# Kernel optimization log

Measured on AMD Instinct MI355X. Metric: run time of the kernel, lower is better.

The kernel has to match this reference:

```python
import jax, jax.numpy as jnp
import numpy as np


def _conv3d(x, w):
    # x: [N, C, D, H, W], w: [O, I, K, K, K] -> [N, O, D', H', W'] VALID conv
    return jax.lax.conv_general_dilated(
        x, w, window_strides=(1, 1, 1), padding='VALID',
        dimension_numbers=('NCDHW', 'OIDHW', 'NCDHW'))


def conv4d(x, w):
    # x: [B, C, D1, D2, D3, D4]; w: [O, I, K1, K2, K3, K4]
    # Decompose 4D conv as a sum over K1 taps of 3D convs; the sliced D1
    # window is folded into the batch dimension so XLA's 3D conv does the work.
    B, C, D1, D2, D3, D4 = x.shape
    O, I, K1, K2, K3, K4 = w.shape
    D1o = D1 - K1 + 1
    out = None
    for i in range(K1):  # small fixed loop over kernel taps (K1=3)
        xs = jax.lax.dynamic_slice_in_dim(x, i, D1o, axis=2)      # [B,C,D1o,D2,D3,D4]
        xs = xs.transpose(0, 2, 1, 3, 4, 5).reshape(B * D1o, C, D2, D3, D4)
        y = _conv3d(xs, w[:, :, i])                                # [B*D1o,O,d2,d3,d4]
        out = y if out is None else out + y
    d2, d3, d4 = out.shape[2], out.shape[3], out.shape[4]
    out = out.reshape(B, D1o, O, d2, d3, d4).transpose(0, 2, 1, 3, 4, 5)
    return out  # [B, O, D1o, d2, d3, d4]


def setup_inputs() -> dict:
    key = jax.random.key(0)
    k1, k2 = jax.random.split(key)
    pic_in = jax.random.normal(k1, (2, 16, 8, 8, 64, 64), dtype=jnp.float32)
    # convNd weight: [out_channels, in_channels, K, K, K, K], no bias
    weight = jax.random.normal(k2, (32, 16, 3, 3, 3, 3), dtype=jnp.float32) * 0.05
    return {"pic_in": pic_in, "weight": weight}


def reference(pic_in, weight):
    # ConvKernel.forward: 4D conv (stride 1, padding 0, no bias) + ReLU
    return jax.nn.relu(conv4d(pic_in, weight))
```

## Files before the change

### kernel.cpp

```cpp
#include <hip/hip_runtime.h>


typedef __attribute__((ext_vector_type(8))) __bf16 bf16x8;
typedef __attribute__((ext_vector_type(16))) float f32x16;

#define CSTRIDE 262144

#define WT_OFF 0
#define XB_OFF 131072
#define BUF_STRIDE 12544

typedef __attribute__((address_space(1))) const unsigned int gu32;
typedef __attribute__((address_space(3))) unsigned int lu32;

__device__ __forceinline__ void async_cp16(const void* g, void* l) {
  __builtin_amdgcn_global_load_lds((gu32*)g, (lu32*)l, 16, 0, 0);
}

__global__ __launch_bounds__(256) void prep(const float* __restrict__ x,
                                            const float* __restrict__ w,
                                            unsigned char* __restrict__ ws) {
  int blk = blockIdx.x;
  if (blk < 512) {
    __bf16* xb = (__bf16*)(ws + XB_OFF);
    int n = blk * 256 + threadIdx.x;
    int cg = n & 15;
    int d3 = (n >> 4) & 63;
    int d2 = (n >> 10) & 7;
    int d1 = (n >> 13) & 7;
    int b = n >> 16;
    const float* gx =
        x + ((((b * 16) * 8 + d1) * 8 + d2) * 64 + d3) * 64 + cg * 4;
    float4 v[16];
#pragma unroll
    for (int c = 0; c < 16; ++c) v[c] = *(const float4*)(gx + (size_t)c * CSTRIDE);
    __bf16* row = xb + ((((b * 8 + d1) * 8 + d2) * 64 + d3) * 1024);
#pragma unroll
    for (int ch = 0; ch < 2; ++ch) {
#pragma unroll
      for (int j = 0; j < 4; ++j) {
        bf16x8 o;
#pragma unroll
        for (int cc = 0; cc < 8; ++cc)
          o[cc] = (__bf16)(((const float*)&v[ch * 8 + cc])[j]);
        *(bf16x8*)(row + ch * 512 + (cg * 4 + j) * 8) = o;
      }
    }
  } else {
    int o = blk - 512;
    __bf16* wT = (__bf16*)(ws + WT_OFF);
#pragma unroll
    for (int base = 0; base < 1296; base += 256) {
      int idx = base + threadIdx.x;
      if (idx < 1296) {
        int c = idx / 81, t = idx % 81;
        wT[t * 512 + o * 16 + c] = (__bf16)w[o * 1296 + idx];
      }
    }
  }
}

__global__ __launch_bounds__(256, 4) void conv_mfma(
    const unsigned char* __restrict__ ws, float* __restrict__ out) {
  const __bf16* wT = (const __bf16*)(ws + WT_OFF);
  const unsigned char* xb = ws + XB_OFF;

  int bid = blockIdx.x;
  int c3 = bid & 15;
  int t = bid >> 4;
  int e2 = t % 6;
  t /= 6;
  int e1 = t % 6;
  int b = t / 6;
  int r0 = c3 * 4;
  int T3 = (c3 == 15) ? 2 : 4;
  int nchunk = (T3 + 2) * 2;
  int ntiles = T3 >> 1;

  int lane = threadIdx.x & 63;
  int wave = threadIdx.x >> 6;
  int m32 = lane & 31;
  int half = lane >> 5;

  __shared__ __align__(16) unsigned char lds[2 * BUF_STRIDE];

  int ab_off = (wave >> 1) * 2048 + half * 1024 + ((wave & 1) * 32 + m32) * 16;

  f32x16 acc[2];
#pragma unroll
  for (int i = 0; i < 2; ++i)
#pragma unroll
    for (int r = 0; r < 16; ++r) acc[i][r] = 0.f;

  {
    const unsigned char* g =
        xb + (((b * 8 + e1) * 8 + e2) * 64 + r0) * 2048;
#pragma unroll
    for (int j = 0; j < 3; ++j) {
      int ck = j * 4 + wave;
      if (ck < nchunk) async_cp16(g + ck * 1024 + lane * 16, lds + ck * 1024);
    }
  }

  for (int p = 0; p < 9; ++p) {
    __syncthreads();
    const __bf16* wp = wT + p * 4608 + m32 * 16 + half * 8;
    bf16x8 bfr[9];
#pragma unroll
    for (int t9 = 0; t9 < 9; ++t9) bfr[t9] = *(const bf16x8*)(wp + t9 * 512);
    if (p < 8) {
      int np = p + 1;
      int nk1 = np / 3, nk2 = np - nk1 * 3;
      const unsigned char* g =
          xb + (((b * 8 + e1 + nk1) * 8 + e2 + nk2) * 64 + r0) * 2048;
      unsigned char* dst = lds + (np & 1) * BUF_STRIDE;
#pragma unroll
      for (int j = 0; j < 3; ++j) {
        int ck = j * 4 + wave;
        if (ck < nchunk)
          async_cp16(g + ck * 1024 + lane * 16, dst + ck * 1024);
      }
    }
    const unsigned char* abase = lds + (p & 1) * BUF_STRIDE + ab_off;
#pragma unroll
    for (int k3 = 0; k3 < 3; ++k3) {
#pragma unroll
      for (int k4 = 0; k4 < 3; ++k4) {
        bf16x8 bf = bfr[k3 * 3 + k4];
        bf16x8 a0 = *(const bf16x8*)(abase + k3 * 2048 + k4 * 16);
        acc[0] =
            __builtin_amdgcn_mfma_f32_32x32x16_bf16(a0, bf, acc[0], 0, 0, 0);
        if (ntiles == 2) {
          bf16x8 a1 = *(const bf16x8*)(abase + 4096 + k3 * 2048 + k4 * 16);
          acc[1] =
              __builtin_amdgcn_mfma_f32_32x32x16_bf16(a1, bf, acc[1], 0, 0, 0);
        }
      }
    }
  }
  __syncthreads();

  float* scw = (float*)(void*)lds + wave * 1056;
#pragma unroll
  for (int i = 0; i < 2; ++i) {
    if (i >= ntiles) break;
    int tr = (wave >> 1) + 2 * i;
    int th = wave & 1;
#pragma unroll
    for (int r = 0; r < 16; ++r) {
      int m = (r & 3) + 8 * (r >> 2) + 4 * half;
      scw[m * 33 + m32] = acc[i][r];
    }
    int e3 = r0 + tr;
    size_t obase =
        ((((size_t)b * 32) * 6 + e1) * 6 + e2) * 3844 + (size_t)e3 * 62;
    int e4 = th * 32 + m32;
#pragma unroll
    for (int it = 0; it < 16; ++it) {
      int o = it * 2 + half;
      float v = fmaxf(scw[m32 * 33 + o], 0.f);
      if (e4 < 62) out[obase + (size_t)o * 138384 + e4] = v;
    }
  }
}

extern "C" void kernel_launch(void* const* d_in, const int* in_sizes, int n_in,
                              void* d_out, int out_size, void* d_ws,
                              size_t ws_size, hipStream_t stream) {
  const float* x = (const float*)d_in[0];
  const float* w = (const float*)d_in[1];
  float* out = (float*)d_out;
  unsigned char* ws = (unsigned char*)d_ws;
  prep<<<dim3(544), dim3(256), 0, stream>>>(x, w, ws);
  conv_mfma<<<dim3(1152), dim3(256), 0, stream>>>(ws, out);
}
```

Baseline: 116.5 us.

## Replace LDS double-buffered staging with single-wave blocks using register row reuse

The conv kernel drops the async global-to-LDS double buffering and its per-tap block barriers. It now launches one-wave blocks, each computing four output rows for half the width. A sliding window of six input rows is loaded straight from global memory into registers and reused across the three k3 taps, feeding four accumulators. This removes LDS traffic and synchronisation but relies on L1/L2 for input reuse and leaves global-load latency without explicit prefetch. The last row tile now also computes and reads past its valid rows before discarding them.

```diff
diff --git a/kernel.cpp b/kernel.cpp
--- a/kernel.cpp
+++ b/kernel.cpp
@@ -8,14 +8,6 @@
 
 #define WT_OFF 0
 #define XB_OFF 131072
-#define BUF_STRIDE 12544
-
-typedef __attribute__((address_space(1))) const unsigned int gu32;
-typedef __attribute__((address_space(3))) unsigned int lu32;
-
-__device__ __forceinline__ void async_cp16(const void* g, void* l) {
-  __builtin_amdgcn_global_load_lds((gu32*)g, (lu32*)l, 16, 0, 0);
-}
 
 __global__ __launch_bounds__(256) void prep(const float* __restrict__ x,
                                             const float* __restrict__ w,
@@ -33,7 +25,8 @@
         x + ((((b * 16) * 8 + d1) * 8 + d2) * 64 + d3) * 64 + cg * 4;
     float4 v[16];
 #pragma unroll
-    for (int c = 0; c < 16; ++c) v[c] = *(const float4*)(gx + (size_t)c * CSTRIDE);
+    for (int c = 0; c < 16; ++c)
+      v[c] = *(const float4*)(gx + (size_t)c * CSTRIDE);
     __bf16* row = xb + ((((b * 8 + d1) * 8 + d2) * 64 + d3) * 1024);
 #pragma unroll
     for (int ch = 0; ch < 2; ++ch) {
@@ -60,106 +53,78 @@
   }
 }
 
-__global__ __launch_bounds__(256, 4) void conv_mfma(
+__global__ __launch_bounds__(64, 3) void conv_mfma(
     const unsigned char* __restrict__ ws, float* __restrict__ out) {
-  const __bf16* wT = (const __bf16*)(ws + WT_OFF);
-  const unsigned char* xb = ws + XB_OFF;
+  const unsigned char* wTb = ws + WT_OFF;
+  const unsigned char* xbb = ws + XB_OFF;
 
   int bid = blockIdx.x;
   int c3 = bid & 15;
-  int t = bid >> 4;
+  int th = (bid >> 4) & 1;
+  int t = bid >> 5;
   int e2 = t % 6;
   t /= 6;
   int e1 = t % 6;
   int b = t / 6;
   int r0 = c3 * 4;
-  int T3 = (c3 == 15) ? 2 : 4;
-  int nchunk = (T3 + 2) * 2;
-  int ntiles = T3 >> 1;
 
-  int lane = threadIdx.x & 63;
-  int wave = threadIdx.x >> 6;
+  int lane = threadIdx.x;
   int m32 = lane & 31;
   int half = lane >> 5;
 
-  __shared__ __align__(16) unsigned char lds[2 * BUF_STRIDE];
+  int aoff = half * 1024 + (th * 32 + m32) * 16;
+  int woff = m32 * 32 + half * 16;
 
-  int ab_off = (wave >> 1) * 2048 + half * 1024 + ((wave & 1) * 32 + m32) * 16;
-
-  f32x16 acc[2];
+  f32x16 acc[4];
 #pragma unroll
-  for (int i = 0; i < 2; ++i)
+  for (int i = 0; i < 4; ++i)
 #pragma unroll
     for (int r = 0; r < 16; ++r) acc[i][r] = 0.f;
 
-  {
-    const unsigned char* g =
-        xb + (((b * 8 + e1) * 8 + e2) * 64 + r0) * 2048;
-#pragma unroll
-    for (int j = 0; j < 3; ++j) {
-      int ck = j * 4 + wave;
-      if (ck < nchunk) async_cp16(g + ck * 1024 + lane * 16, lds + ck * 1024);
-    }
-  }
-
-  for (int p = 0; p < 9; ++p) {
-    __syncthreads();
-    const __bf16* wp = wT + p * 4608 + m32 * 16 + half * 8;
-    bf16x8 bfr[9];
-#pragma unroll
-    for (int t9 = 0; t9 < 9; ++t9) bfr[t9] = *(const bf16x8*)(wp + t9 * 512);
-    if (p < 8) {
-      int np = p + 1;
-      int nk1 = np / 3, nk2 = np - nk1 * 3;
-      const unsigned char* g =
-          xb + (((b * 8 + e1 + nk1) * 8 + e2 + nk2) * 64 + r0) * 2048;
-      unsigned char* dst = lds + (np & 1) * BUF_STRIDE;
-#pragma unroll
-      for (int j = 0; j < 3; ++j) {
-        int ck = j * 4 + wave;
-        if (ck < nchunk)
-          async_cp16(g + ck * 1024 + lane * 16, dst + ck * 1024);
-      }
-    }
-    const unsigned char* abase = lds + (p & 1) * BUF_STRIDE + ab_off;
-#pragma unroll
-    for (int k3 = 0; k3 < 3; ++k3) {
+  for (int k1 = 0; k1 < 3; ++k1) {
+    for (int k2 = 0; k2 < 3; ++k2) {
+      const unsigned char* abase =
+          xbb +
+          (size_t)(((b * 8 + e1 + k1) * 8 + e2 + k2) * 64 + r0) * 2048 + aoff;
+      const unsigned char* wbase = wTb + (k1 * 3 + k2) * 9216 + woff;
 #pragma unroll
       for (int k4 = 0; k4 < 3; ++k4) {
-        bf16x8 bf = bfr[k3 * 3 + k4];
-        bf16x8 a0 = *(const bf16x8*)(abase + k3 * 2048 + k4 * 16);
-        acc[0] =
-            __builtin_amdgcn_mfma_f32_32x32x16_bf16(a0, bf, acc[0], 0, 0, 0);
-        if (ntiles == 2) {
-          bf16x8 a1 = *(const bf16x8*)(abase + 4096 + k3 * 2048 + k4 * 16);
-          acc[1] =
-              __builtin_amdgcn_mfma_f32_32x32x16_bf16(a1, bf, acc[1], 0, 0, 0);
+        bf16x8 arow[6];
+#pragma unroll
+        for (int j = 0; j < 6; ++j)
+          arow[j] = *(const bf16x8*)(abase + j * 2048 + k4 * 16);
+#pragma unroll
+        for (int k3 = 0; k3 < 3; ++k3) {
+          bf16x8 bf = *(const bf16x8*)(wbase + (k3 * 3 + k4) * 1024);
+#pragma unroll
+          for (int i = 0; i < 4; ++i)
+            acc[i] = __builtin_amdgcn_mfma_f32_32x32x16_bf16(arow[i + k3], bf,
+                                                             acc[i], 0, 0, 0);
         }
       }
     }
   }
-  __syncthreads();
 
-  float* scw = (float*)(void*)lds + wave * 1056;
+  __shared__ float sc[32 * 33];
+  int e4 = th * 32 + m32;
+  size_t obase_be = ((size_t)b * 32 * 36 + e1 * 6 + e2) * 3844;
 #pragma unroll
-  for (int i = 0; i < 2; ++i) {
-    if (i >= ntiles) break;
-    int tr = (wave >> 1) + 2 * i;
-    int th = wave & 1;
+  for (int i = 0; i < 4; ++i) {
+    int e3 = r0 + i;
+    if (e3 >= 62) break;
+    __syncthreads();
 #pragma unroll
     for (int r = 0; r < 16; ++r) {
       int m = (r & 3) + 8 * (r >> 2) + 4 * half;
-      scw[m * 33 + m32] = acc[i][r];
+      sc[m * 33 + m32] = acc[i][r];
     }
-    int e3 = r0 + tr;
-    size_t obase =
-        ((((size_t)b * 32) * 6 + e1) * 6 + e2) * 3844 + (size_t)e3 * 62;
-    int e4 = th * 32 + m32;
+    __syncthreads();
 #pragma unroll
     for (int it = 0; it < 16; ++it) {
       int o = it * 2 + half;
-      float v = fmaxf(scw[m32 * 33 + o], 0.f);
-      if (e4 < 62) out[obase + (size_t)o * 138384 + e4] = v;
+      float v = fmaxf(sc[m32 * 33 + o], 0.f);
+      if (e4 < 62)
+        out[obase_be + (size_t)o * 138384 + (size_t)e3 * 62 + e4] = v;
     }
   }
 }
@@ -172,5 +137,5 @@
   float* out = (float*)d_out;
   unsigned char* ws = (unsigned char*)d_ws;
   prep<<<dim3(544), dim3(256), 0, stream>>>(x, w, ws);
-  conv_mfma<<<dim3(1152), dim3(256), 0, stream>>>(ws, out);
+  conv_mfma<<<dim3(2 * 6 * 6 * 2 * 16), dim3(64), 0, stream>>>(ws, out);
 }
```

Measured after the change: 127.2 us. 9.2% more time.

## Enlarge conv tile to six output rows and reuse A fragments across k3

Applied to the files above, without the earlier changes.

Each block now computes six d3 output rows instead of four, with three tiles per wave group. Loaded A rows are reused across the three k3 taps through a sliding window, which cuts LDS reads per MFMA. The block-to-work mapping is rewritten (792 blocks, with a 2-row remainder handled by a template specialization), and a separate LDS scratch region is used for the epilogue. Larger LDS and register use lowers the occupancy bound from 4 to 3 blocks per CU.

```diff
diff --git a/kernel.cpp b/kernel.cpp
--- a/kernel.cpp
+++ b/kernel.cpp
@@ -8,7 +8,8 @@
 
 #define WT_OFF 0
 #define XB_OFF 131072
-#define BUF_STRIDE 12544
+#define ABUF 16640
+#define SCR_OFF (2 * ABUF)
 
 typedef __attribute__((address_space(1))) const unsigned int gu32;
 typedef __attribute__((address_space(3))) unsigned int lu32;
@@ -33,7 +34,8 @@
         x + ((((b * 16) * 8 + d1) * 8 + d2) * 64 + d3) * 64 + cg * 4;
     float4 v[16];
 #pragma unroll
-    for (int c = 0; c < 16; ++c) v[c] = *(const float4*)(gx + (size_t)c * CSTRIDE);
+    for (int c = 0; c < 16; ++c)
+      v[c] = *(const float4*)(gx + (size_t)c * CSTRIDE);
     __bf16* row = xb + ((((b * 8 + d1) * 8 + d2) * 64 + d3) * 1024);
 #pragma unroll
     for (int ch = 0; ch < 2; ++ch) {
@@ -60,108 +62,117 @@
   }
 }
 
-__global__ __launch_bounds__(256, 4) void conv_mfma(
-    const unsigned char* __restrict__ ws, float* __restrict__ out) {
-  const __bf16* wT = (const __bf16*)(ws + WT_OFF);
-  const unsigned char* xb = ws + XB_OFF;
-
-  int bid = blockIdx.x;
-  int c3 = bid & 15;
-  int t = bid >> 4;
-  int e2 = t % 6;
-  t /= 6;
-  int e1 = t % 6;
-  int b = t / 6;
-  int r0 = c3 * 4;
-  int T3 = (c3 == 15) ? 2 : 4;
-  int nchunk = (T3 + 2) * 2;
-  int ntiles = T3 >> 1;
-
+template <int NT>
+__device__ __forceinline__ void conv_body(
+    const unsigned char* __restrict__ wTb, const unsigned char* __restrict__ xbb,
+    float* __restrict__ out, unsigned char* lds, int b, int e1, int e2,
+    int r0) {
   int lane = threadIdx.x & 63;
   int wave = threadIdx.x >> 6;
   int m32 = lane & 31;
   int half = lane >> 5;
+  int rg = wave >> 1;
+  int th = wave & 1;
+  int rowbase = rg * NT;
+  const int nck = (NT * 2 + 2) * 2;
 
-  __shared__ __align__(16) unsigned char lds[2 * BUF_STRIDE];
+  int ab_off = half * 1024 + (th * 32 + m32) * 16;
 
-  int ab_off = (wave >> 1) * 2048 + half * 1024 + ((wave & 1) * 32 + m32) * 16;
-
-  f32x16 acc[2];
+  f32x16 acc[NT];
 #pragma unroll
-  for (int i = 0; i < 2; ++i)
+  for (int i = 0; i < NT; ++i)
 #pragma unroll
     for (int r = 0; r < 16; ++r) acc[i][r] = 0.f;
 
   {
     const unsigned char* g =
-        xb + (((b * 8 + e1) * 8 + e2) * 64 + r0) * 2048;
+        xbb + (size_t)(((b * 8 + e1) * 8 + e2) * 64 + r0) * 2048;
 #pragma unroll
-    for (int j = 0; j < 3; ++j) {
+    for (int j = 0; j < 4; ++j) {
       int ck = j * 4 + wave;
-      if (ck < nchunk) async_cp16(g + ck * 1024 + lane * 16, lds + ck * 1024);
+      if (ck < nck) async_cp16(g + ck * 1024 + lane * 16, lds + ck * 1024);
     }
   }
 
   for (int p = 0; p < 9; ++p) {
     __syncthreads();
-    const __bf16* wp = wT + p * 4608 + m32 * 16 + half * 8;
+    const unsigned char* wp = wTb + p * 9216 + m32 * 32 + half * 16;
     bf16x8 bfr[9];
 #pragma unroll
-    for (int t9 = 0; t9 < 9; ++t9) bfr[t9] = *(const bf16x8*)(wp + t9 * 512);
+    for (int t9 = 0; t9 < 9; ++t9)
+      bfr[t9] = *(const bf16x8*)(wp + t9 * 1024);
     if (p < 8) {
       int np = p + 1;
       int nk1 = np / 3, nk2 = np - nk1 * 3;
       const unsigned char* g =
-          xb + (((b * 8 + e1 + nk1) * 8 + e2 + nk2) * 64 + r0) * 2048;
-      unsigned char* dst = lds + (np & 1) * BUF_STRIDE;
+          xbb + (size_t)(((b * 8 + e1 + nk1) * 8 + e2 + nk2) * 64 + r0) * 2048;
+      unsigned char* dst = lds + (np & 1) * ABUF;
 #pragma unroll
-      for (int j = 0; j < 3; ++j) {
+      for (int j = 0; j < 4; ++j) {
         int ck = j * 4 + wave;
-        if (ck < nchunk)
-          async_cp16(g + ck * 1024 + lane * 16, dst + ck * 1024);
+        if (ck < nck) async_cp16(g + ck * 1024 + lane * 16, dst + ck * 1024);
       }
     }
-    const unsigned char* abase = lds + (p & 1) * BUF_STRIDE + ab_off;
+    const unsigned char* abase =
+        lds + (p & 1) * ABUF + rowbase * 2048 + ab_off;
 #pragma unroll
-    for (int k3 = 0; k3 < 3; ++k3) {
+    for (int k4 = 0; k4 < 3; ++k4) {
+      bf16x8 arow[NT + 2];
 #pragma unroll
-      for (int k4 = 0; k4 < 3; ++k4) {
+      for (int j = 0; j < NT + 2; ++j)
+        arow[j] = *(const bf16x8*)(abase + j * 2048 + k4 * 16);
+#pragma unroll
+      for (int k3 = 0; k3 < 3; ++k3) {
         bf16x8 bf = bfr[k3 * 3 + k4];
-        bf16x8 a0 = *(const bf16x8*)(abase + k3 * 2048 + k4 * 16);
-        acc[0] =
-            __builtin_amdgcn_mfma_f32_32x32x16_bf16(a0, bf, acc[0], 0, 0, 0);
-        if (ntiles == 2) {
-          bf16x8 a1 = *(const bf16x8*)(abase + 4096 + k3 * 2048 + k4 * 16);
-          acc[1] =
-              __builtin_amdgcn_mfma_f32_32x32x16_bf16(a1, bf, acc[1], 0, 0, 0);
-        }
+#pragma unroll
+        for (int i = 0; i < NT; ++i)
+          acc[i] = __builtin_amdgcn_mfma_f32_32x32x16_bf16(arow[i + k3], bf,
+                                                           acc[i], 0, 0, 0);
       }
     }
   }
   __syncthreads();
 
-  float* scw = (float*)(void*)lds + wave * 1056;
+  float* sc = (float*)(void*)(lds + SCR_OFF) + wave * 1056;
+  int e4 = th * 32 + m32;
 #pragma unroll
-  for (int i = 0; i < 2; ++i) {
-    if (i >= ntiles) break;
-    int tr = (wave >> 1) + 2 * i;
-    int th = wave & 1;
+  for (int i = 0; i < NT; ++i) {
+    int e3 = r0 + rowbase + i;
 #pragma unroll
     for (int r = 0; r < 16; ++r) {
       int m = (r & 3) + 8 * (r >> 2) + 4 * half;
-      scw[m * 33 + m32] = acc[i][r];
+      sc[m * 33 + m32] = acc[i][r];
     }
-    int e3 = r0 + tr;
     size_t obase =
         ((((size_t)b * 32) * 6 + e1) * 6 + e2) * 3844 + (size_t)e3 * 62;
-    int e4 = th * 32 + m32;
 #pragma unroll
     for (int it = 0; it < 16; ++it) {
       int o = it * 2 + half;
-      float v = fmaxf(scw[m32 * 33 + o], 0.f);
+      float v = fmaxf(sc[m32 * 33 + o], 0.f);
       if (e4 < 62) out[obase + (size_t)o * 138384 + e4] = v;
     }
   }
+}
+
+__global__ __launch_bounds__(256, 3) void conv_mfma(
+    const unsigned char* __restrict__ ws, float* __restrict__ out) {
+  const unsigned char* wTb = ws + WT_OFF;
+  const unsigned char* xbb = ws + XB_OFF;
+
+  __shared__ __align__(16) unsigned char lds[2 * ABUF + 4 * 4224];
+
+  int bid = blockIdx.x;
+  int g = bid % 72;
+  int chunk = bid / 72;
+  int b = g / 36;
+  int e1 = (g / 6) % 6;
+  int e2 = g % 6;
+  int r0 = chunk * 6;
+
+  if (chunk < 10)
+    conv_body<3>(wTb, xbb, out, lds, b, e1, e2, r0);
+  else
+    conv_body<1>(wTb, xbb, out, lds, b, e1, e2, r0);
 }
 
 extern "C" void kernel_launch(void* const* d_in, const int* in_sizes, int n_in,
@@ -172,5 +183,5 @@
   float* out = (float*)d_out;
   unsigned char* ws = (unsigned char*)d_ws;
   prep<<<dim3(544), dim3(256), 0, stream>>>(x, w, ws);
-  conv_mfma<<<dim3(1152), dim3(256), 0, stream>>>(ws, out);
+  conv_mfma<<<dim3(792), dim3(256), 0, stream>>>(ws, out);
 }
```

After: 114.6 us. No clear change (-1.7%).
